# Kernel optimization log

Measured on AMD Instinct MI355X. Metric: run time of the kernel, lower is better.

## Reference

```python
import jax, jax.numpy as jnp
import numpy as np

L, B, S, D, H, F = 4, 8, 512, 512, 8, 2048
KS = (1, 3, 5)
DEPTH = D // H


def causal_conv(x, W, b):
    # x: [B,S,D], W: [k,D,D] (WIO), causal left pad k-1
    k = W.shape[0]
    y = jax.lax.conv_general_dilated(x, W, (1,), [(k - 1, 0)],
                                     dimension_numbers=('NWC', 'WIO', 'NWC'))
    return y + b


def layer_norm(x, g, b, eps=1e-6):
    mu = jnp.mean(x, -1, keepdims=True)
    var = jnp.mean((x - mu) ** 2, -1, keepdims=True)
    return (x - mu) * jax.lax.rsqrt(var + eps) * g + b


def split_heads(t):
    return t.reshape(B, S, H, DEPTH).transpose(0, 2, 1, 3)  # [B,H,S,depth]


def setup_inputs() -> dict:
    key = jax.random.key(0)
    keys = iter(jax.random.split(key, 16))
    rn = lambda shape, s=0.02: jax.random.normal(next(keys), shape, jnp.float32) * s
    inp = {"x": jax.random.normal(next(keys), (B, S, D), jnp.float32)}
    for k in KS:
        inp[f"Wq{k}"] = rn((L, k, D, D))
        inp[f"Wk{k}"] = rn((L, k, D, D))
    inp["bq"] = jnp.zeros((L, 3, D), jnp.float32)
    inp["bk"] = jnp.zeros((L, 3, D), jnp.float32)
    inp["Wv"] = rn((L, 3, 1, D, D))
    inp["bv"] = jnp.zeros((L, 3, D), jnp.float32)
    inp["Wo"] = rn((L, D, D)); inp["bo"] = jnp.zeros((L, D), jnp.float32)
    inp["W1"] = rn((L, D, F)); inp["b1"] = jnp.zeros((L, F), jnp.float32)
    inp["W2"] = rn((L, F, D)); inp["b2"] = jnp.zeros((L, D), jnp.float32)
    inp["ln1_g"] = jnp.ones((L, D), jnp.float32); inp["ln1_b"] = jnp.zeros((L, D), jnp.float32)
    inp["ln2_g"] = jnp.ones((L, D), jnp.float32); inp["ln2_b"] = jnp.zeros((L, D), jnp.float32)
    return inp


def reference(x, Wq1, Wq3, Wq5, Wk1, Wk3, Wk5, bq, bk, Wv, bv, Wo, bo,
              W1, b1, W2, b2, ln1_g, ln1_b, ln2_g, ln2_b):
    # causal look-ahead mask: 1 - band_part(ones, -1, 0), added as mask * -1e9
    neg_mask = (1.0 - jnp.tril(jnp.ones((S, S), jnp.float32))) * -1e9
    scale = 1.0 / jnp.sqrt(jnp.float32(DEPTH))
    Wqs, Wks = (Wq1, Wq3, Wq5), (Wk1, Wk3, Wk5)
    for l in range(L):
        outs = []
        for i in range(len(KS)):
            q = split_heads(causal_conv(x, Wqs[i][l], bq[l, i]))
            k = split_heads(causal_conv(x, Wks[i][l], bk[l, i]))
            v = split_heads(causal_conv(x, Wv[l, i], bv[l, i]))
            logits = jnp.einsum('bhqd,bhkd->bhqk', q, k) * scale + neg_mask
            a = jax.nn.softmax(logits, axis=-1)
            o = jnp.einsum('bhqk,bhkd->bhqd', a, v)
            outs.append(o.transpose(0, 2, 1, 3).reshape(B, S, D))
        attn_out = ((outs[0] + outs[1] + outs[2]) / 3.0) @ Wo[l] + bo[l]
        out1 = layer_norm(attn_out + x, ln1_g[l], ln1_b[l])
        ffn = jax.nn.relu(out1 @ W1[l] + b1[l]) @ W2[l] + b2[l]
        x = layer_norm(ffn + out1, ln2_g[l], ln2_b[l])
    return x
```

## Files before the change

kernel.cpp:

```cpp
#include <hip/hip_runtime.h>
#include <cstdint>
#include <cstddef>

#define Dm 512
#define Sm 512
#define Bm 8
#define Hm 8
#define Fm 2048
#define Mm 4096
#define Lm 4

typedef __bf16 bf16x8 __attribute__((ext_vector_type(8)));
typedef float  fx4    __attribute__((ext_vector_type(4)));
typedef float  fx2    __attribute__((ext_vector_type(2)));
typedef unsigned short u16;
typedef unsigned short u16x4 __attribute__((ext_vector_type(4)));
typedef short s16x8 __attribute__((ext_vector_type(8)));

__device__ __forceinline__ u16 f2b(float f) {
  union { float f; uint32_t u; } v; v.f = f;
  uint32_t u = v.u;
  return (u16)((u + 0x7fffu + ((u >> 16) & 1u)) >> 16);
}
__device__ __forceinline__ float b2f(u16 h) {
  union { uint32_t u; float f; } v; v.u = ((uint32_t)h) << 16;
  return v.f;
}

__device__ __forceinline__ void gload16(const void* g, void* l) {
  __builtin_amdgcn_global_load_lds(
      (const __attribute__((address_space(1))) void*)g,
      (__attribute__((address_space(3))) void*)l, 16, 0, 0);
}

template<int N>
__device__ __forceinline__ void vwait() {
  if constexpr (N == 4)      asm volatile("s_waitcnt vmcnt(4)" ::: "memory");
  else if constexpr (N == 8) asm volatile("s_waitcnt vmcnt(8)" ::: "memory");
  else                       asm volatile("s_waitcnt vmcnt(0)" ::: "memory");
}

__global__ void cast_bf16_kernel(const float* __restrict__ in, u16* __restrict__ out,
                                 u16* __restrict__ zpad) {
  int i = (blockIdx.x * 256 + threadIdx.x) * 4;
  fx4 v = *(const fx4*)(in + i);
  u16x4 o;
  #pragma unroll
  for (int j = 0; j < 4; ++j) o[j] = f2b(v[j]);
  *(u16x4*)(out + i) = o;
  if (blockIdx.x == 0) { zpad[threadIdx.x] = 0; zpad[threadIdx.x + 256] = 0; }
}

__global__ void ln_kernel(const float* __restrict__ in, const float* __restrict__ gam,
                          const float* __restrict__ bet, float* __restrict__ outf,
                          u16* __restrict__ outb) {
  int row = blockIdx.x;
  int t = threadIdx.x;
  const float* x = in + (size_t)row * Dm;
  fx4 v0 = *(const fx4*)(x + t*4);
  fx4 v1 = *(const fx4*)(x + 256 + t*4);
  float s = 0.f, sq = 0.f;
  #pragma unroll
  for (int j = 0; j < 4; ++j) { s += v0[j] + v1[j]; sq += v0[j]*v0[j] + v1[j]*v1[j]; }
  #pragma unroll
  for (int off = 1; off < 64; off <<= 1) { s += __shfl_xor(s, off, 64); sq += __shfl_xor(sq, off, 64); }
  float mu  = s * (1.f/Dm);
  float var = sq * (1.f/Dm) - mu*mu;
  float rstd = rsqrtf(var + 1e-6f);
  fx4 g0 = *(const fx4*)(gam + t*4), g1 = *(const fx4*)(gam + 256 + t*4);
  fx4 b0 = *(const fx4*)(bet + t*4), b1 = *(const fx4*)(bet + 256 + t*4);
  float* of = outf + (size_t)row*Dm;
  u16*   ob = outb + (size_t)row*Dm;
  fx4 y0, y1; u16x4 h0, h1;
  #pragma unroll
  for (int j = 0; j < 4; ++j) {
    y0[j] = (v0[j]-mu)*rstd*g0[j] + b0[j];
    y1[j] = (v1[j]-mu)*rstd*g1[j] + b1[j];
    h0[j] = f2b(y0[j]); h1[j] = f2b(y1[j]);
  }
  *(fx4*)(of + t*4) = y0; *(fx4*)(of + 256 + t*4) = y1;
  *(u16x4*)(ob + t*4) = h0; *(u16x4*)(ob + 256 + t*4) = h1;
}

#define TST 130
__global__ void prep_kernel(u16* __restrict__ packed,
    const float* __restrict__ Wq1, const float* __restrict__ Wq3, const float* __restrict__ Wq5,
    const float* __restrict__ Wk1, const float* __restrict__ Wk3, const float* __restrict__ Wk5,
    const float* __restrict__ Wv,  const float* __restrict__ Wo,
    const float* __restrict__ W1,  const float* __restrict__ W2, int layer) {
  __shared__ float T[64 * TST];
  constexpr int t0[13] = {0,32,128,288,320,416,576,608,640,672,704,832,960};
  int bid = blockIdx.x;
  int seg = 0;
  while (bid >= t0[seg+1]) ++seg;
  int local = bid - t0[seg];
  const float* src; int K, N;
  switch (seg) {
    case 0:  src = Wq1 + (size_t)layer*512*512;   K = 512;  N = 512;  break;
    case 1:  src = Wq3 + (size_t)layer*3*512*512; K = 1536; N = 512;  break;
    case 2:  src = Wq5 + (size_t)layer*5*512*512; K = 2560; N = 512;  break;
    case 3:  src = Wk1 + (size_t)layer*512*512;   K = 512;  N = 512;  break;
    case 4:  src = Wk3 + (size_t)layer*3*512*512; K = 1536; N = 512;  break;
    case 5:  src = Wk5 + (size_t)layer*5*512*512; K = 2560; N = 512;  break;
    case 6:  src = Wv + (size_t)(layer*3+0)*512*512; K = 512; N = 512; break;
    case 7:  src = Wv + (size_t)(layer*3+1)*512*512; K = 512; N = 512; break;
    case 8:  src = Wv + (size_t)(layer*3+2)*512*512; K = 512; N = 512; break;
    case 9:  src = Wo + (size_t)layer*512*512;    K = 512;  N = 512;  break;
    case 10: src = W1 + (size_t)layer*512*2048;   K = 512;  N = 2048; break;
    default: src = W2 + (size_t)layer*2048*512;   K = 2048; N = 512;  break;
  }
  int KT = K >> 6;
  int ntile = local / KT, ktile = local - ntile*KT;
  const float* sb = src + (size_t)(ktile*64)*N + ntile*128;
  int tid = threadIdx.x;
  #pragma unroll
  for (int i = 0; i < 16; ++i) {
    int idx = i*256 + tid;
    int row = idx >> 6, col2 = (idx & 63) * 2;
    fx2 v = *(const fx2*)(sb + (size_t)row*N + col2);
    *(fx2*)(&T[row*TST + col2]) = v;
  }
  __syncthreads();
  u16* dst = packed + ((size_t)bid << 13);
  #pragma unroll
  for (int j = 0; j < 4; ++j) {
    int z = j*256 + tid;
    int row = z >> 3;
    int c = (z & 7) ^ (row & 7);
    s16x8 o;
    #pragma unroll
    for (int e = 0; e < 8; ++e) o[e] = (short)f2b(T[(c*8 + e)*TST + row]);
    *(s16x8*)(dst + z*8) = o;
  }
}

#define GEMM_STEP(IDX, CB, NB, BC, BN, NRv, NW)                                   \
  {                                                                              \
    bool hn = (IDX) + 1 < ntiles;                                                \
    if (hn) {                                                                    \
      stageA(NB);                                                                \
      ++skt; if (skt == KTt) { skt = 0; ++st; }                                  \
      const u16* wtn = WtN + ((size_t)((IDX) + 1) << 13);                        \
      _Pragma("unroll")                                                          \
      for (int kk = 0; kk < 2; ++kk)                                             \
        _Pragma("unroll")                                                        \
        for (int n = 0; n < NRv; ++n) {                                          \
          int row = wn*(NRv*16) + n*16 + r16;                                    \
          BN[kk][n] = *(const bf16x8*)(wtn + (row << 6) + (((kk*4 + g) ^ (row & 7)) << 3)); \
        }                                                                        \
    }                                                                            \
    bf16x8 a_[2][4];                                                             \
    _Pragma("unroll")                                                            \
    for (int kk = 0; kk < 2; ++kk)                                               \
      _Pragma("unroll")                                                          \
      for (int m = 0; m < 4; ++m) {                                              \
        int row = wm*64 + m*16 + r16;                                            \
        a_[kk][m] = *(const bf16x8*)(&As[CB][(row << 6) + (((kk*4 + g) ^ (row & 7)) << 3)]); \
      }                                                                          \
    __builtin_amdgcn_s_setprio(1);                                               \
    _Pragma("unroll")                                                            \
    for (int kk = 0; kk < 2; ++kk)                                               \
      _Pragma("unroll")                                                          \
      for (int m = 0; m < 4; ++m)                                                \
        _Pragma("unroll")                                                        \
        for (int n = 0; n < NRv; ++n)                                            \
          acc[m][n] = __builtin_amdgcn_mfma_f32_16x16x32_bf16(a_[kk][m], BC[kk][n], acc[m][n], 0, 0, 0); \
    __builtin_amdgcn_s_setprio(0);                                               \
    vwait<2*NRv>();                                                              \
    __builtin_amdgcn_s_barrier();                                                \
  }

__global__ __launch_bounds__(256, 2) void conv_all(const u16* __restrict__ xb,
    const u16* __restrict__ packed,
    const float* __restrict__ bq, const float* __restrict__ bk, const float* __restrict__ bv,
    u16* __restrict__ qb, u16* __restrict__ kb, u16* __restrict__ vT, int layer,
    const u16* __restrict__ zpad) {
  __shared__ __align__(16) u16 As[2][8192];
  constexpr int t0c[9]   = {0,32,128,288,320,416,576,608,640};
  constexpr int tapsc[9] = {1,3,5,1,3,5,1,1,1};
  constexpr int order[9] = {2,5,1,4,0,3,6,7,8};
  int bid = blockIdx.x;
  int unit = order[bid >> 7];
  int local = bid & 127;
  int mtile = local >> 2, ntile = local & 3;
  int taps = tapsc[unit];
  int brow = mtile * 128, bcol = ntile * 128;
  int tid = threadIdx.x, lane = tid & 63, wid = tid >> 6;
  int wm = wid >> 1, wn = wid & 1;
  int r16 = lane & 15, g = lane >> 4;
  const u16* WtN = packed + ((size_t)(t0c[unit] + ntile * taps * 8) << 13);
  fx4 acc[4][4] = {};
  int ntiles = taps * 8;
  const int KTt = 8;
  int st = 0, skt = 0;
  auto stageA = [&](int bufi) {
    int shift = taps - 1 - st;
    int c0 = skt << 6;
    #pragma unroll
    for (int j = 0; j < 4; ++j) {
      int zb = wid*256 + j*64;
      int zz = zb + lane;
      int row = zz >> 3, c = (zz & 7) ^ (row & 7);
      int s = (brow + row) & (Sm - 1);
      const u16* src = (s >= shift) ? (xb + (size_t)(brow + row - shift)*Dm + c0 + c*8) : zpad;
      gload16(src, &As[bufi][zb * 8]);
    }
  };
  bf16x8 bA[2][4], bB[2][4];
  stageA(0);
  ++skt; if (skt == KTt) { skt = 0; ++st; }
  #pragma unroll
  for (int kk = 0; kk < 2; ++kk)
    #pragma unroll
    for (int n = 0; n < 4; ++n) {
      int row = wn*64 + n*16 + r16;
      bA[kk][n] = *(const bf16x8*)(WtN + (row << 6) + (((kk*4 + g) ^ (row & 7)) << 3));
    }
  __syncthreads();
  for (int base = 0; base < ntiles; base += 2) {
    GEMM_STEP(base,     0, 1, bA, bB, 4, 2)
    GEMM_STEP(base + 1, 1, 0, bB, bA, 4, 2)
  }
  const float* bias; u16* outp;
  if (unit < 3)      { bias = bq + (size_t)(layer*3 + unit)*Dm;   outp = qb + (size_t)unit*Mm*Dm; }
  else if (unit < 6) { bias = bk + (size_t)(layer*3 + unit-3)*Dm; outp = kb + (size_t)(unit-3)*Mm*Dm; }
  else               { bias = bv + (size_t)(layer*3 + unit-6)*Dm; outp = vT + ((size_t)(unit-6) << 21); }
  if (unit < 6) {
    #pragma unroll
    for (int m = 0; m < 4; ++m) {
      int row0 = brow + wm*64 + m*16 + g*4;
      #pragma unroll
      for (int n = 0; n < 4; ++n) {
        int col = bcol + wn*64 + n*16 + r16;
        float bv_ = bias[col];
        #pragma unroll
        for (int r = 0; r < 4; ++r)
          outp[(size_t)(row0 + r)*Dm + col] = f2b(acc[m][n][r] + bv_);
      }
    }
  } else {
    #pragma unroll
    for (int m = 0; m < 4; ++m) {
      int row0 = brow + wm*64 + m*16 + g*4;
      int bidx = row0 >> 9, spos = row0 & 511;
      #pragma unroll
      for (int n = 0; n < 4; ++n) {
        int col = bcol + wn*64 + n*16 + r16;
        int hh = col >> 6, dd = col & 63;
        float bv_ = bias[col];
        u16x4 pk;
        #pragma unroll
        for (int r = 0; r < 4; ++r) pk[r] = f2b(acc[m][n][r] + bv_);
        *(u16x4*)(outp + (((size_t)(bidx*8 + hh)*64 + dd) << 9) + spos) = pk;
      }
    }
  }
}

template<int MODE, int BMt, int WN, bool CAUSAL>
__device__ __forceinline__ void gemm_core(const u16* __restrict__ A, int lda, int Ktap, int taps,
    const u16* __restrict__ Wt, const float* __restrict__ bias, const float* __restrict__ res,
    u16* __restrict__ outb, float* __restrict__ outf, int N, const u16* __restrict__ zpad) {
  constexpr int NR = 128 / (16 * WN);
  constexpr int AD = BMt / 32;
  __shared__ __align__(16) u16 As[2][BMt * 64];
  int tid = threadIdx.x, lane = tid & 63, wid = tid >> 6;
  int wm = (WN == 2) ? (wid >> 1) : 0;
  int wn = (WN == 2) ? (wid & 1) : wid;
  int r16 = lane & 15, g = lane >> 4;
  int brow = blockIdx.x * BMt, bcol = blockIdx.y * 128;
  const int KTt = Ktap >> 6;
  const u16* WtN = Wt + ((size_t)(blockIdx.y * taps * KTt) << 13);
  fx4 acc[4][NR] = {};
  int ntiles = taps * KTt;
  int st = 0, skt = 0;
  auto stageA = [&](int bufi) {
    int shift = taps - 1 - st;
    int c0 = skt << 6;
    #pragma unroll
    for (int j = 0; j < AD; ++j) {
      int zb = wid*(BMt*2) + j*64;
      int zz = zb + lane;
      int row = zz >> 3, c = (zz & 7) ^ (row & 7);
      const u16* src;
      if (CAUSAL) {
        int s = (brow + row) & (Sm - 1);
        src = (s >= shift) ? (A + (size_t)(brow + row - shift)*lda + c0 + c*8) : zpad;
      } else {
        src = A + (size_t)(brow + row)*lda + c0 + c*8;
      }
      gload16(src, &As[bufi][zb * 8]);
    }
  };
  bf16x8 bA[2][NR], bB[2][NR];
  stageA(0);
  ++skt; if (skt == KTt) { skt = 0; ++st; }
  #pragma unroll
  for (int kk = 0; kk < 2; ++kk)
    #pragma unroll
    for (int n = 0; n < NR; ++n) {
      int row = wn*(NR*16) + n*16 + r16;
      bA[kk][n] = *(const bf16x8*)(WtN + (row << 6) + (((kk*4 + g) ^ (row & 7)) << 3));
    }
  __syncthreads();
  for (int base = 0; base < ntiles; base += 2) {
    GEMM_STEP(base,     0, 1, bA, bB, NR, WN)
    GEMM_STEP(base + 1, 1, 0, bB, bA, NR, WN)
  }
  #pragma unroll
  for (int m = 0; m < 4; ++m) {
    int row0 = brow + wm*64 + m*16 + g*4;
    #pragma unroll
    for (int n = 0; n < NR; ++n) {
      int col = bcol + wn*(NR*16) + n*16 + r16;
      float bv_ = bias[col];
      #pragma unroll
      for (int r = 0; r < 4; ++r) {
        size_t idx = (size_t)(row0 + r)*N + col;
        float v = acc[m][n][r] + bv_;
        if (MODE == 0)      outb[idx] = f2b(v);
        else if (MODE == 1) outb[idx] = f2b(fmaxf(v, 0.f));
        else                outf[idx] = v + res[idx];
      }
    }
  }
}

template<int MODE, int BMt, int WN, int LB>
__global__ __launch_bounds__(256, LB) void gemm_dense(const u16* __restrict__ A, int lda, int K,
    const u16* __restrict__ Wt, const float* __restrict__ bias, const float* __restrict__ res,
    u16* __restrict__ outb, float* __restrict__ outf, int N) {
  gemm_core<MODE, BMt, WN, false>(A, lda, K, 1, Wt, bias, res, outb, outf, N, nullptr);
}

__global__ __launch_bounds__(256, 2) void gemm_wo(const u16* __restrict__ o3,
    const u16* __restrict__ Wt, const float* __restrict__ bias, const float* __restrict__ res,
    float* __restrict__ outf) {
  __shared__ __align__(16) u16 As[2][4096];
  int tid = threadIdx.x, lane = tid & 63, wid = tid >> 6;
  int wn = wid;
  int r16 = lane & 15, g = lane >> 4;
  int brow = blockIdx.x * 64, bcol = blockIdx.y * 128;
  const u16* WtN = Wt + ((size_t)(blockIdx.y * 8) << 13);
  fx4 acc[4][2] = {};
  auto stage = [&](int bufi, int kt) {
    int c0 = kt << 6;
    #pragma unroll
    for (int j = 0; j < 2; ++j) {
      int z = j*256 + tid;
      int row = z >> 3, c = (z & 7) ^ (row & 7);
      const u16* p = o3 + (size_t)(brow + row)*Dm + c0 + c*8;
      s16x8 va = *(const s16x8*)(p);
      s16x8 vb = *(const s16x8*)(p + (size_t)Mm*Dm);
      s16x8 vc = *(const s16x8*)(p + (size_t)2*Mm*Dm);
      s16x8 o;
      #pragma unroll
      for (int e = 0; e < 8; ++e)
        o[e] = (short)f2b((b2f((u16)va[e]) + b2f((u16)vb[e]) + b2f((u16)vc[e])) * (1.f/3.f));
      *(s16x8*)(&As[bufi][z * 8]) = o;
    }
  };
  auto loadB = [&](bf16x8 (&bf)[2][2], int kt) {
    const u16* wt = WtN + ((size_t)kt << 13);
    #pragma unroll
    for (int kk = 0; kk < 2; ++kk)
      #pragma unroll
      for (int n = 0; n < 2; ++n) {
        int row = wn*32 + n*16 + r16;
        bf[kk][n] = *(const bf16x8*)(wt + (row << 6) + (((kk*4 + g) ^ (row & 7)) << 3));
      }
  };
  bf16x8 bC[2][2], bN[2][2];
  stage(0, 0);
  loadB(bC, 0);
  __syncthreads();
  #define WOSTEP(IDX, CB, BC_, BN_)                                               \
    {                                                                             \
      if ((IDX) + 1 < 8) { stage((CB) ^ 1, (IDX) + 1); loadB(BN_, (IDX) + 1); }   \
      bf16x8 a_[2][4];                                                            \
      _Pragma("unroll")                                                           \
      for (int kk = 0; kk < 2; ++kk)                                              \
        _Pragma("unroll")                                                         \
        for (int m = 0; m < 4; ++m) {                                             \
          int row = m*16 + r16;                                                   \
          a_[kk][m] = *(const bf16x8*)(&As[CB][(row << 6) + (((kk*4 + g) ^ (row & 7)) << 3)]); \
        }                                                                         \
      _Pragma("unroll")                                                           \
      for (int kk = 0; kk < 2; ++kk)                                              \
        _Pragma("unroll")                                                         \
        for (int m = 0; m < 4; ++m)                                               \
          _Pragma("unroll")                                                       \
          for (int n = 0; n < 2; ++n)                                             \
            acc[m][n] = __builtin_amdgcn_mfma_f32_16x16x32_bf16(a_[kk][m], BC_[kk][n], acc[m][n], 0, 0, 0); \
      __syncthreads();                                                            \
    }
  for (int base = 0; base < 8; base += 2) {
    WOSTEP(base,     0, bC, bN)
    WOSTEP(base + 1, 1, bN, bC)
  }
  #undef WOSTEP
  #pragma unroll
  for (int m = 0; m < 4; ++m) {
    int row0 = brow + m*16 + g*4;
    #pragma unroll
    for (int n = 0; n < 2; ++n) {
      int col = bcol + wn*32 + n*16 + r16;
      float bv_ = bias[col];
      #pragma unroll
      for (int r = 0; r < 4; ++r) {
        size_t idx = (size_t)(row0 + r)*Dm + col;
        outf[idx] = acc[m][n][r] + bv_ + res[idx];
      }
    }
  }
}

__global__ __launch_bounds__(256, 3) void attn_kernel(const u16* __restrict__ qb,
    const u16* __restrict__ kb, const u16* __restrict__ vTb, u16* __restrict__ ob) {
  __shared__ __align__(16) u16 Ks[2][4096];
  __shared__ __align__(16) u16 Vs[2][4096];
  __shared__ __align__(16) u16 Ps[4][1024];
  int a = blockIdx.x, bh = blockIdx.y, br = blockIdx.z;
  int b = bh >> 3, h = bh & 7;
  const u16* q  = qb + (size_t)br*Mm*Dm;
  const u16* k  = kb + (size_t)br*Mm*Dm;
  const u16* vT = vTb + (((size_t)br << 21) + ((size_t)bh << 15));
  u16* o = ob + (size_t)br*Mm*Dm;
  int tid = threadIdx.x, lane = tid & 63, wid = tid >> 6;
  int r16 = lane & 15, g = lane >> 4;
  size_t rowbase = (size_t)b * Sm;
  int qt[2] = {7 - a, a};
  int nkt = qt[0] + 1;

  bf16x8 qa[2][2];
  #pragma unroll
  for (int t2 = 0; t2 < 2; ++t2)
    #pragma unroll
    for (int c = 0; c < 2; ++c)
      qa[t2][c] = *(const bf16x8*)(q + (rowbase + qt[t2]*64 + wid*16 + r16)*Dm + h*64 + c*32 + g*8);

  float m_[2][4], l_[2][4];
  fx4 accO[2][4] = {};
  #pragma unroll
  for (int t2 = 0; t2 < 2; ++t2)
    #pragma unroll
    for (int r = 0; r < 4; ++r) { m_[t2][r] = -3.0e38f; l_[t2][r] = 0.f; }

  auto stage = [&](int kt, int bufi) {
    #pragma unroll
    for (int it = 0; it < 2; ++it) {
      int zb = wid*128 + it*64;
      int zz = zb + lane;
      int row = zz >> 3, c = (zz & 7) ^ (row & 7);
      gload16(k + (rowbase + kt*64 + row)*Dm + h*64 + c*8, &Ks[bufi][zb * 8]);
      gload16(vT + ((size_t)row << 9) + kt*64 + c*8, &Vs[bufi][zb * 8]);
    }
  };
  stage(0, 0);
  __syncthreads();

  for (int kt = 0; kt < nkt; ++kt) {
    int cur = kt & 1;
    if (kt + 1 < nkt) stage(kt + 1, cur ^ 1);
    #pragma unroll
    for (int t2 = 0; t2 < 2; ++t2) {
      if (t2 == 0 || kt <= qt[1]) {
        fx4 sacc[4] = {};
        #pragma unroll
        for (int c = 0; c < 2; ++c)
          #pragma unroll
          for (int n = 0; n < 4; ++n) {
            int row = n*16 + r16;
            bf16x8 kf = *(const bf16x8*)(&Ks[cur][(row << 6) + (((c*4 + g) ^ (row & 7)) << 3)]);
            sacc[n] = __builtin_amdgcn_mfma_f32_16x16x32_bf16(qa[t2][c], kf, sacc[n], 0, 0, 0);
          }
        float sv[4][4];
        bool diag = (kt == qt[t2]);
        #pragma unroll
        for (int n = 0; n < 4; ++n)
          #pragma unroll
          for (int r = 0; r < 4; ++r) {
            float s = sacc[n][r] * 0.125f;
            if (diag && (n*16 + r16 > wid*16 + g*4 + r)) s = -3.0e38f;
            sv[n][r] = s;
          }
        #pragma unroll
        for (int r = 0; r < 4; ++r) {
          float rm = fmaxf(fmaxf(sv[0][r], sv[1][r]), fmaxf(sv[2][r], sv[3][r]));
          #pragma unroll
          for (int off = 1; off < 16; off <<= 1) rm = fmaxf(rm, __shfl_xor(rm, off, 64));
          float mnew = fmaxf(m_[t2][r], rm);
          float corr = __expf(m_[t2][r] - mnew);
          m_[t2][r] = mnew;
          float rs = 0.f;
          #pragma unroll
          for (int n = 0; n < 4; ++n) { float p = __expf(sv[n][r] - mnew); sv[n][r] = p; rs += p; }
          #pragma unroll
          for (int off = 1; off < 16; off <<= 1) rs += __shfl_xor(rs, off, 64);
          l_[t2][r] = l_[t2][r]*corr + rs;
          #pragma unroll
          for (int n = 0; n < 4; ++n) accO[t2][n][r] *= corr;
        }
        #pragma unroll
        for (int n = 0; n < 4; ++n)
          #pragma unroll
          for (int r = 0; r < 4; ++r) {
            int qq = g*4 + r;
            Ps[wid][(qq << 6) + (((n*2 + (r16 >> 3)) ^ (qq & 7)) << 3) + (r16 & 7)] = f2b(sv[n][r]);
          }
        #pragma unroll
        for (int kk = 0; kk < 2; ++kk) {
          bf16x8 pa = *(const bf16x8*)(&Ps[wid][(r16 << 6) + (((kk*4 + g) ^ (r16 & 7)) << 3)]);
          #pragma unroll
          for (int n = 0; n < 4; ++n) {
            int row = n*16 + r16;
            bf16x8 vf = *(const bf16x8*)(&Vs[cur][(row << 6) + (((kk*4 + g) ^ (row & 7)) << 3)]);
            accO[t2][n] = __builtin_amdgcn_mfma_f32_16x16x32_bf16(pa, vf, accO[t2][n], 0, 0, 0);
          }
        }
      }
    }
    __syncthreads();
  }
  #pragma unroll
  for (int t2 = 0; t2 < 2; ++t2)
    #pragma unroll
    for (int n = 0; n < 4; ++n)
      #pragma unroll
      for (int r = 0; r < 4; ++r) {
        int qrow = qt[t2]*64 + wid*16 + g*4 + r;
        o[(rowbase + qrow)*Dm + h*64 + n*16 + r16] = f2b(accO[t2][n][r] / l_[t2][r]);
      }
}

extern "C" void kernel_launch(void* const* d_in, const int* in_sizes, int n_in,
                              void* d_out, int out_size, void* d_ws, size_t ws_size,
                              hipStream_t stream) {
  const float* x_in = (const float*)d_in[0];
  const float* Wq1 = (const float*)d_in[1];
  const float* Wk1 = (const float*)d_in[2];
  const float* Wq3 = (const float*)d_in[3];
  const float* Wk3 = (const float*)d_in[4];
  const float* Wq5 = (const float*)d_in[5];
  const float* Wk5 = (const float*)d_in[6];
  const float* bq  = (const float*)d_in[7];
  const float* bk  = (const float*)d_in[8];
  const float* Wv  = (const float*)d_in[9];
  const float* bv  = (const float*)d_in[10];
  const float* Wo  = (const float*)d_in[11];
  const float* bo  = (const float*)d_in[12];
  const float* W1  = (const float*)d_in[13];
  const float* b1  = (const float*)d_in[14];
  const float* W2  = (const float*)d_in[15];
  const float* b2  = (const float*)d_in[16];
  const float* ln1g = (const float*)d_in[17];
  const float* ln1b = (const float*)d_in[18];
  const float* ln2g = (const float*)d_in[19];
  const float* ln2b = (const float*)d_in[20];

  char* ws = (char*)d_ws;
  size_t off = 0;
  auto alloc = [&](size_t bytes) { void* p = ws + off; off += (bytes + 255) & ~(size_t)255; return p; };
  float* x_f32 = (float*)alloc((size_t)Mm*Dm*4);
  u16*   xb    = (u16*)  alloc((size_t)Mm*Dm*2);
  u16*   qbuf  = (u16*)  alloc((size_t)3*Mm*Dm*2);
  u16*   kbuf  = (u16*)  alloc((size_t)3*Mm*Dm*2);
  u16*   vT    = (u16*)  alloc((size_t)3*Mm*Dm*2);
  u16*   obuf  = (u16*)  alloc((size_t)3*Mm*Dm*2);
  float* pre   = (float*)alloc((size_t)Mm*Dm*4);
  float* out1f = (float*)alloc((size_t)Mm*Dm*4);
  u16*   out1b = (u16*)  alloc((size_t)Mm*Dm*2);
  u16*   midb  = (u16*)  alloc((size_t)Mm*Fm*2);
  u16*   packed= (u16*)  alloc((size_t)960*8192*2);
  u16*   zpad  = (u16*)  alloc(1024);

  cast_bf16_kernel<<<2048, 256, 0, stream>>>(x_in, xb, zpad);
  for (int l = 0; l < Lm; ++l) {
    const float* xs = (l == 0) ? x_in : x_f32;
    prep_kernel<<<960, 256, 0, stream>>>(packed, Wq1, Wq3, Wq5, Wk1, Wk3, Wk5,
                                         Wv, Wo, W1, W2, l);
    conv_all<<<1152, 256, 0, stream>>>(
        xb, packed, bq, bk, bv, qbuf, kbuf, vT, l, zpad);
    attn_kernel<<<dim3(4, 64, 3), 256, 0, stream>>>(qbuf, kbuf, vT, obuf);
    gemm_wo<<<dim3(64, 4), 256, 0, stream>>>(
        obuf, packed + ((size_t)672 << 13), bo + (size_t)l*Dm, xs, pre);
    ln_kernel<<<4096, 64, 0, stream>>>(pre, ln1g + (size_t)l*Dm, ln1b + (size_t)l*Dm, out1f, out1b);
    gemm_dense<1, 128, 2, 2><<<dim3(32, 16), 256, 0, stream>>>(
        out1b, 512, 512, packed + ((size_t)704 << 13), b1 + (size_t)l*Fm, nullptr, midb, nullptr, 2048);
    gemm_dense<2, 64, 4, 3><<<dim3(64, 4), 256, 0, stream>>>(
        midb, 2048, 2048, packed + ((size_t)832 << 13), b2 + (size_t)l*Dm, out1f, nullptr, pre, 512);
    float* lnout = (l == Lm-1) ? (float*)d_out : x_f32;
    ln_kernel<<<4096, 64, 0, stream>>>(pre, ln2g + (size_t)l*Dm, ln2b + (size_t)l*Dm, lnout, xb);
  }
}
```

Before: 621.4 us.

## Double the K-step per pipeline stage in conv and dense GEMMs

```diff
diff --git a/kernel.cpp b/kernel.cpp
--- a/kernel.cpp
+++ b/kernel.cpp
@@ -35,9 +35,12 @@
 
 template<int N>
 __device__ __forceinline__ void vwait() {
-  if constexpr (N == 4)      asm volatile("s_waitcnt vmcnt(4)" ::: "memory");
-  else if constexpr (N == 8) asm volatile("s_waitcnt vmcnt(8)" ::: "memory");
-  else                       asm volatile("s_waitcnt vmcnt(0)" ::: "memory");
+  if constexpr (N == 4)       asm volatile("s_waitcnt vmcnt(4)"  ::: "memory");
+  else if constexpr (N == 8)  asm volatile("s_waitcnt vmcnt(8)"  ::: "memory");
+  else if constexpr (N == 12) asm volatile("s_waitcnt vmcnt(12)" ::: "memory");
+  else if constexpr (N == 16) asm volatile("s_waitcnt vmcnt(16)" ::: "memory");
+  else if constexpr (N == 24) asm volatile("s_waitcnt vmcnt(24)" ::: "memory");
+  else                        asm volatile("s_waitcnt vmcnt(0)"  ::: "memory");
 }
 
 __global__ void cast_bf16_kernel(const float* __restrict__ in, u16* __restrict__ out,
@@ -134,29 +137,38 @@
   }
 }
 
-#define GEMM_STEP(IDX, CB, NB, BC, BN, NRv, NW)                                   \
+#define GEMM_STEP2(IDX, CB, BPC, BPN, NRv, SS, AA, HB)                            \
   {                                                                              \
     bool hn = (IDX) + 1 < ntiles;                                                \
+    const u16* wt1 = WtN + ((size_t)(2*(IDX)+1) << 13);                          \
+    bf16x8 b1_[2][NRv];                                                          \
+    _Pragma("unroll")                                                            \
+    for (int kk = 0; kk < 2; ++kk)                                               \
+      _Pragma("unroll")                                                          \
+      for (int n = 0; n < NRv; ++n) {                                            \
+        int row = wn*(NRv*16) + n*16 + r16;                                      \
+        b1_[kk][n] = *(const bf16x8*)(wt1 + (row << 6) + (((kk*4 + g) ^ (row & 7)) << 3)); \
+      }                                                                          \
     if (hn) {                                                                    \
-      stageA(NB);                                                                \
-      ++skt; if (skt == KTt) { skt = 0; ++st; }                                  \
-      const u16* wtn = WtN + ((size_t)((IDX) + 1) << 13);                        \
+      stageA2((CB) ^ 1);                                                         \
+      const u16* wt0n = WtN + ((size_t)(2*(IDX)+2) << 13);                       \
       _Pragma("unroll")                                                          \
       for (int kk = 0; kk < 2; ++kk)                                             \
         _Pragma("unroll")                                                        \
         for (int n = 0; n < NRv; ++n) {                                          \
           int row = wn*(NRv*16) + n*16 + r16;                                    \
-          BN[kk][n] = *(const bf16x8*)(wtn + (row << 6) + (((kk*4 + g) ^ (row & 7)) << 3)); \
+          BPN[kk][n] = *(const bf16x8*)(wt0n + (row << 6) + (((kk*4 + g) ^ (row & 7)) << 3)); \
         }                                                                        \
     }                                                                            \
-    bf16x8 a_[2][4];                                                             \
+    bf16x8 a0_[2][4];                                                            \
     _Pragma("unroll")                                                            \
     for (int kk = 0; kk < 2; ++kk)                                               \
       _Pragma("unroll")                                                          \
       for (int m = 0; m < 4; ++m) {                                              \
         int row = wm*64 + m*16 + r16;                                            \
-        a_[kk][m] = *(const bf16x8*)(&As[CB][(row << 6) + (((kk*4 + g) ^ (row & 7)) << 3)]); \
+        a0_[kk][m] = *(const bf16x8*)(&As[CB][(row << 6) + (((kk*4 + g) ^ (row & 7)) << 3)]); \
       }                                                                          \
+    if (hn) vwait<2*(SS) + (AA)>(); else vwait<(SS)>();                          \
     __builtin_amdgcn_s_setprio(1);                                               \
     _Pragma("unroll")                                                            \
     for (int kk = 0; kk < 2; ++kk)                                               \
@@ -164,10 +176,27 @@
       for (int m = 0; m < 4; ++m)                                                \
         _Pragma("unroll")                                                        \
         for (int n = 0; n < NRv; ++n)                                            \
-          acc[m][n] = __builtin_amdgcn_mfma_f32_16x16x32_bf16(a_[kk][m], BC[kk][n], acc[m][n], 0, 0, 0); \
+          acc[m][n] = __builtin_amdgcn_mfma_f32_16x16x32_bf16(a0_[kk][m], BPC[kk][n], acc[m][n], 0, 0, 0); \
     __builtin_amdgcn_s_setprio(0);                                               \
-    vwait<2*NRv>();                                                              \
-    __builtin_amdgcn_s_barrier();                                                \
+    bf16x8 a1_[2][4];                                                            \
+    _Pragma("unroll")                                                            \
+    for (int kk = 0; kk < 2; ++kk)                                               \
+      _Pragma("unroll")                                                          \
+      for (int m = 0; m < 4; ++m) {                                              \
+        int row = wm*64 + m*16 + r16;                                            \
+        a1_[kk][m] = *(const bf16x8*)(&As[CB][(HB) + (row << 6) + (((kk*4 + g) ^ (row & 7)) << 3)]); \
+      }                                                                          \
+    if (hn) vwait<(SS) + (AA)>(); else vwait<0>();                               \
+    __builtin_amdgcn_s_setprio(1);                                               \
+    _Pragma("unroll")                                                            \
+    for (int kk = 0; kk < 2; ++kk)                                               \
+      _Pragma("unroll")                                                          \
+      for (int m = 0; m < 4; ++m)                                                \
+        _Pragma("unroll")                                                        \
+        for (int n = 0; n < NRv; ++n)                                            \
+          acc[m][n] = __builtin_amdgcn_mfma_f32_16x16x32_bf16(a1_[kk][m], b1_[kk][n], acc[m][n], 0, 0, 0); \
+    __builtin_amdgcn_s_setprio(0);                                               \
+    if (hn) { vwait<(SS)>(); __builtin_amdgcn_s_barrier(); }                     \
   }
 
 __global__ __launch_bounds__(256, 2) void conv_all(const u16* __restrict__ xb,
@@ -175,7 +204,7 @@
     const float* __restrict__ bq, const float* __restrict__ bk, const float* __restrict__ bv,
     u16* __restrict__ qb, u16* __restrict__ kb, u16* __restrict__ vT, int layer,
     const u16* __restrict__ zpad) {
-  __shared__ __align__(16) u16 As[2][8192];
+  __shared__ __align__(16) u16 As[2][16384];
   constexpr int t0c[9]   = {0,32,128,288,320,416,576,608,640};
   constexpr int tapsc[9] = {1,3,5,1,3,5,1,1,1};
   constexpr int order[9] = {2,5,1,4,0,3,6,7,8};
@@ -190,25 +219,27 @@
   int r16 = lane & 15, g = lane >> 4;
   const u16* WtN = packed + ((size_t)(t0c[unit] + ntile * taps * 8) << 13);
   fx4 acc[4][4] = {};
-  int ntiles = taps * 8;
-  const int KTt = 8;
+  int ntiles = taps * 4;
   int st = 0, skt = 0;
-  auto stageA = [&](int bufi) {
+  auto stageA2 = [&](int bufi) {
     int shift = taps - 1 - st;
-    int c0 = skt << 6;
-    #pragma unroll
-    for (int j = 0; j < 4; ++j) {
-      int zb = wid*256 + j*64;
-      int zz = zb + lane;
-      int row = zz >> 3, c = (zz & 7) ^ (row & 7);
-      int s = (brow + row) & (Sm - 1);
-      const u16* src = (s >= shift) ? (xb + (size_t)(brow + row - shift)*Dm + c0 + c*8) : zpad;
-      gload16(src, &As[bufi][zb * 8]);
-    }
+    #pragma unroll
+    for (int h = 0; h < 2; ++h) {
+      int c0 = skt*128 + h*64;
+      #pragma unroll
+      for (int j = 0; j < 4; ++j) {
+        int zb = wid*256 + j*64;
+        int zz = zb + lane;
+        int row = zz >> 3, c = (zz & 7) ^ (row & 7);
+        int s = (brow + row) & (Sm - 1);
+        const u16* src = (s >= shift) ? (xb + (size_t)(brow + row - shift)*Dm + c0 + c*8) : zpad;
+        gload16(src, &As[bufi][h*8192 + zb*8]);
+      }
+    }
+    ++skt; if (skt == 4) { skt = 0; ++st; }
   };
   bf16x8 bA[2][4], bB[2][4];
-  stageA(0);
-  ++skt; if (skt == KTt) { skt = 0; ++st; }
+  stageA2(0);
   #pragma unroll
   for (int kk = 0; kk < 2; ++kk)
     #pragma unroll
@@ -218,8 +249,8 @@
     }
   __syncthreads();
   for (int base = 0; base < ntiles; base += 2) {
-    GEMM_STEP(base,     0, 1, bA, bB, 4, 2)
-    GEMM_STEP(base + 1, 1, 0, bB, bA, 4, 2)
+    GEMM_STEP2(base,     0, bA, bB, 4, 8, 8, 8192)
+    GEMM_STEP2(base + 1, 1, bB, bA, 4, 8, 8, 8192)
   }
   const float* bias; u16* outp;
   if (unit < 3)      { bias = bq + (size_t)(layer*3 + unit)*Dm;   outp = qb + (size_t)unit*Mm*Dm; }
@@ -257,44 +288,40 @@
   }
 }
 
-template<int MODE, int BMt, int WN, bool CAUSAL>
-__device__ __forceinline__ void gemm_core(const u16* __restrict__ A, int lda, int Ktap, int taps,
+template<int MODE, int BMt, int WN>
+__device__ __forceinline__ void gemm_core(const u16* __restrict__ A, int lda, int Ktap,
     const u16* __restrict__ Wt, const float* __restrict__ bias, const float* __restrict__ res,
-    u16* __restrict__ outb, float* __restrict__ outf, int N, const u16* __restrict__ zpad) {
+    u16* __restrict__ outb, float* __restrict__ outf, int N) {
   constexpr int NR = 128 / (16 * WN);
   constexpr int AD = BMt / 32;
-  __shared__ __align__(16) u16 As[2][BMt * 64];
+  constexpr int HALF = BMt * 64;
+  __shared__ __align__(16) u16 As[2][2 * HALF];
   int tid = threadIdx.x, lane = tid & 63, wid = tid >> 6;
   int wm = (WN == 2) ? (wid >> 1) : 0;
   int wn = (WN == 2) ? (wid & 1) : wid;
   int r16 = lane & 15, g = lane >> 4;
   int brow = blockIdx.x * BMt, bcol = blockIdx.y * 128;
   const int KTt = Ktap >> 6;
-  const u16* WtN = Wt + ((size_t)(blockIdx.y * taps * KTt) << 13);
+  const u16* WtN = Wt + ((size_t)(blockIdx.y * KTt) << 13);
   fx4 acc[4][NR] = {};
-  int ntiles = taps * KTt;
-  int st = 0, skt = 0;
-  auto stageA = [&](int bufi) {
-    int shift = taps - 1 - st;
-    int c0 = skt << 6;
-    #pragma unroll
-    for (int j = 0; j < AD; ++j) {
-      int zb = wid*(BMt*2) + j*64;
-      int zz = zb + lane;
-      int row = zz >> 3, c = (zz & 7) ^ (row & 7);
-      const u16* src;
-      if (CAUSAL) {
-        int s = (brow + row) & (Sm - 1);
-        src = (s >= shift) ? (A + (size_t)(brow + row - shift)*lda + c0 + c*8) : zpad;
-      } else {
-        src = A + (size_t)(brow + row)*lda + c0 + c*8;
-      }
-      gload16(src, &As[bufi][zb * 8]);
-    }
+  int ntiles = KTt >> 1;
+  int skt = 0;
+  auto stageA2 = [&](int bufi) {
+    #pragma unroll
+    for (int h = 0; h < 2; ++h) {
+      int c0 = skt*128 + h*64;
+      #pragma unroll
+      for (int j = 0; j < AD; ++j) {
+        int zb = wid*(BMt*2) + j*64;
+        int zz = zb + lane;
+        int row = zz >> 3, c = (zz & 7) ^ (row & 7);
+        gload16(A + (size_t)(brow + row)*lda + c0 + c*8, &As[bufi][h*HALF + zb*8]);
+      }
+    }
+    ++skt;
   };
   bf16x8 bA[2][NR], bB[2][NR];
-  stageA(0);
-  ++skt; if (skt == KTt) { skt = 0; ++st; }
+  stageA2(0);
   #pragma unroll
   for (int kk = 0; kk < 2; ++kk)
     #pragma unroll
@@ -304,8 +331,8 @@
     }
   __syncthreads();
   for (int base = 0; base < ntiles; base += 2) {
-    GEMM_STEP(base,     0, 1, bA, bB, NR, WN)
-    GEMM_STEP(base + 1, 1, 0, bB, bA, NR, WN)
+    GEMM_STEP2(base,     0, bA, bB, NR, 2*NR, 2*AD, HALF)
+    GEMM_STEP2(base + 1, 1, bB, bA, NR, 2*NR, 2*AD, HALF)
   }
   #pragma unroll
   for (int m = 0; m < 4; ++m) {
@@ -330,7 +357,7 @@
 __global__ __launch_bounds__(256, LB) void gemm_dense(const u16* __restrict__ A, int lda, int K,
     const u16* __restrict__ Wt, const float* __restrict__ bias, const float* __restrict__ res,
     u16* __restrict__ outb, float* __restrict__ outf, int N) {
-  gemm_core<MODE, BMt, WN, false>(A, lda, K, 1, Wt, bias, res, outb, outf, N, nullptr);
+  gemm_core<MODE, BMt, WN>(A, lda, K, Wt, bias, res, outb, outf, N);
 }
 
 __global__ __launch_bounds__(256, 2) void gemm_wo(const u16* __restrict__ o3,
@@ -587,7 +614,7 @@
     ln_kernel<<<4096, 64, 0, stream>>>(pre, ln1g + (size_t)l*Dm, ln1b + (size_t)l*Dm, out1f, out1b);
     gemm_dense<1, 128, 2, 2><<<dim3(32, 16), 256, 0, stream>>>(
         out1b, 512, 512, packed + ((size_t)704 << 13), b1 + (size_t)l*Fm, nullptr, midb, nullptr, 2048);
-    gemm_dense<2, 64, 4, 3><<<dim3(64, 4), 256, 0, stream>>>(
+    gemm_dense<2, 64, 4, 2><<<dim3(64, 4), 256, 0, stream>>>(
         midb, 2048, 2048, packed + ((size_t)832 << 13), b2 + (size_t)l*Dm, out1f, nullptr, pre, 512);
     float* lnout = (l == Lm-1) ? (float*)d_out : x_f32;
     ln_kernel<<<4096, 64, 0, stream>>>(pre, ln2g + (size_t)l*Dm, ln2b + (size_t)l*Dm, lnout, xb);
```

Result: slower. 751.7 us (+21.0%).

## Load conv A operand directly into registers instead of staging through LDS

Applied to the files above, without the earlier changes.

```diff
diff --git a/kernel.cpp b/kernel.cpp
--- a/kernel.cpp
+++ b/kernel.cpp
@@ -35,9 +35,10 @@
 
 template<int N>
 __device__ __forceinline__ void vwait() {
-  if constexpr (N == 4)      asm volatile("s_waitcnt vmcnt(4)" ::: "memory");
-  else if constexpr (N == 8) asm volatile("s_waitcnt vmcnt(8)" ::: "memory");
-  else                       asm volatile("s_waitcnt vmcnt(0)" ::: "memory");
+  if constexpr (N == 4)       asm volatile("s_waitcnt vmcnt(4)"  ::: "memory");
+  else if constexpr (N == 8)  asm volatile("s_waitcnt vmcnt(8)"  ::: "memory");
+  else if constexpr (N == 16) asm volatile("s_waitcnt vmcnt(16)" ::: "memory");
+  else                        asm volatile("s_waitcnt vmcnt(0)"  ::: "memory");
 }
 
 __global__ void cast_bf16_kernel(const float* __restrict__ in, u16* __restrict__ out,
@@ -170,12 +171,51 @@
     __builtin_amdgcn_s_barrier();                                                \
   }
 
+#define CSTEP(IDX, AC, BC, AN, BN)                                               \
+  {                                                                              \
+    bool hn = (IDX) + 1 < ntiles;                                                \
+    if (hn) {                                                                    \
+      int nidx = (IDX) + 1;                                                      \
+      int nst = nidx >> 3, nsk = nidx & 7;                                       \
+      int shift = taps - 1 - nst;                                                \
+      _Pragma("unroll")                                                          \
+      for (int kk = 0; kk < 2; ++kk)                                             \
+        _Pragma("unroll")                                                        \
+        for (int m = 0; m < 4; ++m) {                                            \
+          int row = brow + wm*64 + m*16 + r16;                                   \
+          int s = row & (Sm - 1);                                                \
+          const u16* srcp = (s >= shift)                                         \
+              ? (xb + (size_t)(row - shift)*Dm + nsk*64 + kk*32 + g*8) : zpad;   \
+          AN[kk][m] = *(const bf16x8*)srcp;                                      \
+        }                                                                        \
+      const u16* wtn = WtN + ((size_t)nidx << 13);                               \
+      _Pragma("unroll")                                                          \
+      for (int kk = 0; kk < 2; ++kk)                                             \
+        _Pragma("unroll")                                                        \
+        for (int n = 0; n < 4; ++n) {                                            \
+          int row = wn*64 + n*16 + r16;                                          \
+          BN[kk][n] = *(const bf16x8*)(wtn + (row << 6) + (((kk*4 + g) ^ (row & 7)) << 3)); \
+        }                                                                        \
+      vwait<16>();                                                               \
+    } else {                                                                     \
+      vwait<0>();                                                                \
+    }                                                                            \
+    __builtin_amdgcn_s_setprio(1);                                               \
+    _Pragma("unroll")                                                            \
+    for (int kk = 0; kk < 2; ++kk)                                               \
+      _Pragma("unroll")                                                          \
+      for (int m = 0; m < 4; ++m)                                                \
+        _Pragma("unroll")                                                        \
+        for (int n = 0; n < 4; ++n)                                              \
+          acc[m][n] = __builtin_amdgcn_mfma_f32_16x16x32_bf16(AC[kk][m], BC[kk][n], acc[m][n], 0, 0, 0); \
+    __builtin_amdgcn_s_setprio(0);                                               \
+  }
+
 __global__ __launch_bounds__(256, 2) void conv_all(const u16* __restrict__ xb,
     const u16* __restrict__ packed,
     const float* __restrict__ bq, const float* __restrict__ bk, const float* __restrict__ bv,
     u16* __restrict__ qb, u16* __restrict__ kb, u16* __restrict__ vT, int layer,
     const u16* __restrict__ zpad) {
-  __shared__ __align__(16) u16 As[2][8192];
   constexpr int t0c[9]   = {0,32,128,288,320,416,576,608,640};
   constexpr int tapsc[9] = {1,3,5,1,3,5,1,1,1};
   constexpr int order[9] = {2,5,1,4,0,3,6,7,8};
@@ -191,35 +231,31 @@
   const u16* WtN = packed + ((size_t)(t0c[unit] + ntile * taps * 8) << 13);
   fx4 acc[4][4] = {};
   int ntiles = taps * 8;
-  const int KTt = 8;
-  int st = 0, skt = 0;
-  auto stageA = [&](int bufi) {
-    int shift = taps - 1 - st;
-    int c0 = skt << 6;
-    #pragma unroll
-    for (int j = 0; j < 4; ++j) {
-      int zb = wid*256 + j*64;
-      int zz = zb + lane;
-      int row = zz >> 3, c = (zz & 7) ^ (row & 7);
-      int s = (brow + row) & (Sm - 1);
-      const u16* src = (s >= shift) ? (xb + (size_t)(brow + row - shift)*Dm + c0 + c*8) : zpad;
-      gload16(src, &As[bufi][zb * 8]);
-    }
-  };
-  bf16x8 bA[2][4], bB[2][4];
-  stageA(0);
-  ++skt; if (skt == KTt) { skt = 0; ++st; }
-  #pragma unroll
-  for (int kk = 0; kk < 2; ++kk)
-    #pragma unroll
-    for (int n = 0; n < 4; ++n) {
-      int row = wn*64 + n*16 + r16;
-      bA[kk][n] = *(const bf16x8*)(WtN + (row << 6) + (((kk*4 + g) ^ (row & 7)) << 3));
-    }
-  __syncthreads();
+
+  bf16x8 aA[2][4], aB[2][4], bA[2][4], bB[2][4];
+  {
+    int shift = taps - 1;
+    #pragma unroll
+    for (int kk = 0; kk < 2; ++kk)
+      #pragma unroll
+      for (int m = 0; m < 4; ++m) {
+        int row = brow + wm*64 + m*16 + r16;
+        int s = row & (Sm - 1);
+        const u16* srcp = (s >= shift)
+            ? (xb + (size_t)(row - shift)*Dm + kk*32 + g*8) : zpad;
+        aA[kk][m] = *(const bf16x8*)srcp;
+      }
+    #pragma unroll
+    for (int kk = 0; kk < 2; ++kk)
+      #pragma unroll
+      for (int n = 0; n < 4; ++n) {
+        int row = wn*64 + n*16 + r16;
+        bA[kk][n] = *(const bf16x8*)(WtN + (row << 6) + (((kk*4 + g) ^ (row & 7)) << 3));
+      }
+  }
   for (int base = 0; base < ntiles; base += 2) {
-    GEMM_STEP(base,     0, 1, bA, bB, 4, 2)
-    GEMM_STEP(base + 1, 1, 0, bB, bA, 4, 2)
+    CSTEP(base,     aA, bA, aB, bB)
+    CSTEP(base + 1, aB, bB, aA, bA)
   }
   const float* bias; u16* outp;
   if (unit < 3)      { bias = bq + (size_t)(layer*3 + unit)*Dm;   outp = qb + (size_t)unit*Mm*Dm; }
```

After: 847.5 us. 36.4% more time.
